# Performance work log

Hardware: AMD Instinct MI355X
Metric: run time of the kernel (lower is better)

Reference implementation:

```python
import jax, jax.numpy as jnp
import numpy as np

# dims: M=512 new tokens, N=2048 model dim, D=128 head dim, H=16 heads,
# L=4096 cache length, P=2048 cache write offset

def setup_inputs() -> dict:
    key = jax.random.key(0)
    k0, k1, k2, k3 = jax.random.split(key, 4)
    M, N, D, L = 512, 2048, 128, 4096
    X = jax.random.normal(k0, (M, N), jnp.float32)
    # scale weights ~1/sqrt(N) so projections have unit-ish scale
    W_qkv = jax.random.normal(k1, (N, 3 * N), jnp.float32) * (N ** -0.5)
    H = N // D
    cache_K = jax.random.normal(k2, (H, L, D), jnp.float32)
    # realistic cache state: keys stored in cache are RMS-normalized
    cache_K = cache_K * jax.lax.rsqrt(jnp.mean(cache_K * cache_K, axis=-1, keepdims=True))
    cache_V = jax.random.normal(k3, (H, L, D), jnp.float32)
    return {"X": X, "W_qkv": W_qkv, "cache_K": cache_K, "cache_V": cache_V, "P": 2048}


def reference(X, W_qkv, cache_K, cache_V, P):
    M = X.shape[0]
    H, L, D = cache_K.shape
    qkv = X @ W_qkv                              # [M, 3N]
    q, k, v = jnp.split(qkv, 3, axis=-1)         # each [M, N]
    q = q.reshape(M, H, D).transpose(1, 0, 2)    # [H, M, D]
    k = k.reshape(M, H, D).transpose(1, 0, 2)
    v = v.reshape(M, H, D).transpose(1, 0, 2)
    # RMS-style normalization (no learned gain, no eps in original)
    q = q * jax.lax.rsqrt(jnp.mean(q * q, axis=-1, keepdims=True))
    k = k * jax.lax.rsqrt(jnp.mean(k * k, axis=-1, keepdims=True))
    # scatter-update into KV cache at position P
    Kc = jax.lax.dynamic_update_slice(cache_K, k, (0, P, 0))  # [H, L, D]
    Vc = jax.lax.dynamic_update_slice(cache_V, v, (0, P, 0))
    # unmasked, unscaled attention over the full cache (faithful to original:
    # plain exp/sum, no max-subtraction, no 1/sqrt(D))
    scores = jnp.einsum('hmd,hld->hml', q, Kc)   # [H, M, L]
    w = jnp.exp(scores)
    w = w / jnp.sum(w, axis=-1, keepdims=True)
    out = jnp.einsum('hml,hld->hmd', w, Vc)      # [H, M, D]
    return out.transpose(1, 0, 2).reshape(M, H * D)
```

## Files before the change

### kernel.cpp

```cpp
#include <hip/hip_runtime.h>
#include <math.h>

typedef _Float16 half_t;
typedef _Float16 half8 __attribute__((ext_vector_type(8)));
typedef _Float16 half4_t __attribute__((ext_vector_type(4)));
typedef _Float16 half2_t __attribute__((ext_vector_type(2)));
typedef float floatx4 __attribute__((ext_vector_type(4)));

#define M_TOK 512
#define N_DIM 2048
#define D_HEAD 128
#define H_HEADS 16
#define L_CACHE 4096
#define THREE_N 6144
#define NCHUNK 8
#define LCHUNK 512

__global__ __launch_bounds__(256) void prep_kernel(const float* __restrict__ cK,
                                                   const float* __restrict__ cV,
                                                   const float* __restrict__ W,
                                                   const float* __restrict__ X,
                                                   const int* __restrict__ Pp,
                                                   half_t* __restrict__ K16,
                                                   half_t* __restrict__ V16T,
                                                   half_t* __restrict__ W16T,
                                                   half_t* __restrict__ X16) {
    __shared__ half_t tile[64 * 66];
    int b = blockIdx.x;
    int t = threadIdx.x;

    if (b < 4096) {
        int l0 = (b & 255) * 16;
        const int P = *Pp;
        if (l0 >= P && l0 + 16 <= P + M_TOK) return;
        size_t i = (size_t)b * 2048 + t * 4;
        float4 v0 = *(const float4*)(cK + i);
        float4 v1 = *(const float4*)(cK + i + 1024);
        half4_t h0 = {(half_t)v0.x, (half_t)v0.y, (half_t)v0.z, (half_t)v0.w};
        half4_t h1 = {(half_t)v1.x, (half_t)v1.y, (half_t)v1.z, (half_t)v1.w};
        *(half4_t*)(K16 + i) = h0;
        *(half4_t*)(K16 + i + 1024) = h1;
        return;
    }
    b -= 4096;
    if (b < 512) {
        size_t i = (size_t)b * 2048 + t * 4;
        float4 v0 = *(const float4*)(X + i);
        float4 v1 = *(const float4*)(X + i + 1024);
        half4_t h0 = {(half_t)v0.x, (half_t)v0.y, (half_t)v0.z, (half_t)v0.w};
        half4_t h1 = {(half_t)v1.x, (half_t)v1.y, (half_t)v1.z, (half_t)v1.w};
        *(half4_t*)(X16 + i) = h0;
        *(half4_t*)(X16 + i + 1024) = h1;
        return;
    }
    b -= 512;
    if (b < 2048) {
        int h = b >> 7;
        int rem = b & 127;
        int lt = rem >> 1, dt = rem & 1;
        int l0 = lt * 64, d0 = dt * 64;
        const int P = *Pp;
        if (l0 >= P && l0 + 64 <= P + M_TOK) return;
        {
            int l = t >> 2, c0 = (t & 3) * 16;
            const float* src = cV + ((size_t)h * L_CACHE + l0 + l) * D_HEAD + d0 + c0;
            float4 v[4];
#pragma unroll
            for (int j = 0; j < 4; ++j) v[j] = *(const float4*)(src + j * 4);
#pragma unroll
            for (int j = 0; j < 4; ++j) {
                tile[(c0 + j * 4 + 0) * 66 + l] = (half_t)v[j].x;
                tile[(c0 + j * 4 + 1) * 66 + l] = (half_t)v[j].y;
                tile[(c0 + j * 4 + 2) * 66 + l] = (half_t)v[j].z;
                tile[(c0 + j * 4 + 3) * 66 + l] = (half_t)v[j].w;
            }
        }
        __syncthreads();
        {
            int d = t >> 2, lg = (t & 3) * 16;
            half_t* dst = V16T + ((size_t)h * D_HEAD + d0 + d) * L_CACHE + l0 + lg;
            *(half8*)(dst) = *(half8*)&tile[d * 66 + lg];
            *(half8*)(dst + 8) = *(half8*)&tile[d * 66 + lg + 8];
        }
        return;
    }
    b -= 2048;
    {
        int n0 = (b % 96) * 64, k0 = (b / 96) * 64;
        {
            int k = t >> 2, c0 = (t & 3) * 16;
            const float* src = W + (size_t)(k0 + k) * THREE_N + n0 + c0;
            float4 v[4];
#pragma unroll
            for (int j = 0; j < 4; ++j) v[j] = *(const float4*)(src + j * 4);
#pragma unroll
            for (int j = 0; j < 4; ++j) {
                tile[(c0 + j * 4 + 0) * 66 + k] = (half_t)v[j].x;
                tile[(c0 + j * 4 + 1) * 66 + k] = (half_t)v[j].y;
                tile[(c0 + j * 4 + 2) * 66 + k] = (half_t)v[j].z;
                tile[(c0 + j * 4 + 3) * 66 + k] = (half_t)v[j].w;
            }
        }
        __syncthreads();
        {
            int n = t >> 2, kg = (t & 3) * 16;
            half_t* dst = W16T + (size_t)(n0 + n) * N_DIM + k0 + kg;
            *(half8*)(dst) = *(half8*)&tile[n * 66 + kg];
            *(half8*)(dst + 8) = *(half8*)&tile[n * 66 + kg + 8];
        }
    }
}

__global__ __launch_bounds__(256) void gemm_fused_kernel(const half_t* __restrict__ X16,
                                                         const half_t* __restrict__ W16T,
                                                         const int* __restrict__ Pp,
                                                         half_t* __restrict__ Q16,
                                                         half_t* __restrict__ K16,
                                                         half_t* __restrict__ V16T) {
    __shared__ half_t As[64 * 72];
    __shared__ half_t Bs[128 * 72];
    __shared__ half_t Vt[128 * 72];
    __shared__ float ssbuf[4][32];
    const int t = threadIdx.x;
    const int wid = t >> 6, lane = t & 63;
    const int quad = lane >> 4, ln = lane & 15;
    const int bx = blockIdx.x, by = blockIdx.y;
    const int m0 = by * 64, n0 = bx * 128;
    const int wm = (wid >> 1) * 32, wn = (wid & 1) * 64;

    floatx4 acc[2][4] = {};

    const int ar = t >> 3, ag = (t & 7) * 8;
    const int br = t >> 3, bg = (t & 7) * 8;

    for (int k0 = 0; k0 < N_DIM; k0 += 64) {
        __syncthreads();
#pragma unroll
        for (int p = 0; p < 2; ++p) {
            int r = ar + p * 32;
            *(half8*)&As[r * 72 + ag] =
                *(const half8*)(X16 + (size_t)(m0 + r) * N_DIM + k0 + ag);
        }
#pragma unroll
        for (int p = 0; p < 4; ++p) {
            int r = br + p * 32;
            *(half8*)&Bs[r * 72 + bg] =
                *(const half8*)(W16T + (size_t)(n0 + r) * N_DIM + k0 + bg);
        }
        __syncthreads();
#pragma unroll
        for (int kt = 0; kt < 2; ++kt) {
            half8 a[2], b[4];
#pragma unroll
            for (int i = 0; i < 2; ++i)
                a[i] = *(half8*)&As[(wm + i * 16 + ln) * 72 + kt * 32 + quad * 8];
#pragma unroll
            for (int j = 0; j < 4; ++j)
                b[j] = *(half8*)&Bs[(wn + j * 16 + ln) * 72 + kt * 32 + quad * 8];
#pragma unroll
            for (int i = 0; i < 2; ++i)
#pragma unroll
                for (int j = 0; j < 4; ++j)
                    acc[i][j] = __builtin_amdgcn_mfma_f32_16x16x32_f16(a[i], b[j], acc[i][j], 0, 0, 0);
        }
    }

    const int seg = bx >> 4, h = bx & 15;
    const int P = *Pp;

    if (seg < 2) {
        float ss[2][4], scale[2][4];
#pragma unroll
        for (int i = 0; i < 2; ++i)
#pragma unroll
            for (int r = 0; r < 4; ++r) {
                float s = 0.f;
#pragma unroll
                for (int j = 0; j < 4; ++j) s += acc[i][j][r] * acc[i][j][r];
#pragma unroll
                for (int msk = 1; msk < 16; msk <<= 1) s += __shfl_xor(s, msk, 64);
                ss[i][r] = s;
            }
        if (ln == 0) {
#pragma unroll
            for (int i = 0; i < 2; ++i)
#pragma unroll
                for (int r = 0; r < 4; ++r)
                    ssbuf[wid][i * 16 + quad * 4 + r] = ss[i][r];
        }
        __syncthreads();
#pragma unroll
        for (int i = 0; i < 2; ++i)
#pragma unroll
            for (int r = 0; r < 4; ++r)
                scale[i][r] =
                    rsqrtf((ss[i][r] + ssbuf[wid ^ 1][i * 16 + quad * 4 + r]) * (1.0f / 128.0f));
#pragma unroll
        for (int i = 0; i < 2; ++i) {
            int mbase = m0 + wm + i * 16 + quad * 4;
#pragma unroll
            for (int j = 0; j < 4; ++j) {
                int col = wn + j * 16 + ln;
#pragma unroll
                for (int r = 0; r < 4; ++r) {
                    int m = mbase + r;
                    half_t val = (half_t)(acc[i][j][r] * scale[i][r]);
                    if (seg == 0)
                        Q16[((size_t)h * M_TOK + m) * D_HEAD + col] = val;
                    else
                        K16[((size_t)h * L_CACHE + P + m) * D_HEAD + col] = val;
                }
            }
        }
    } else {
#pragma unroll
        for (int i = 0; i < 2; ++i) {
            int mbase = wm + i * 16 + quad * 4;
#pragma unroll
            for (int j = 0; j < 4; ++j) {
                int d = wn + j * 16 + ln;
#pragma unroll
                for (int r = 0; r < 4; ++r)
                    Vt[d * 72 + mbase + r] = (half_t)acc[i][j][r];
            }
        }
        __syncthreads();
#pragma unroll
        for (int p = 0; p < 4; ++p) {
            int s = p * 256 + t;
            int d = s >> 3, sg = s & 7;
            *(half8*)(V16T + ((size_t)h * D_HEAD + d) * L_CACHE + P + m0 + sg * 8) =
                *(half8*)&Vt[d * 72 + sg * 8];
        }
    }
}

__global__ __launch_bounds__(256, 4) void attn_partial_kernel(const half_t* __restrict__ Q16,
                                                              const half_t* __restrict__ K16,
                                                              const half_t* __restrict__ V16T,
                                                              half_t* __restrict__ Opart,
                                                              float* __restrict__ mstat,
                                                              float* __restrict__ lstat) {
    __shared__ half_t Ks[64 * 128];
    __shared__ half_t Vs[128 * 64];
    __shared__ half_t Ps[4 * 16 * 64];
    const int t = threadIdx.x, w = t >> 6, lane = t & 63;
    const int quad = lane >> 4, ln = lane & 15;

    const int bid = blockIdx.x;
    const int xcd = bid & 7, slot = bid >> 3;
    const int pair = (xcd << 4) | (slot >> 3);
    const int h = pair & 15, c = pair >> 4, mi = slot & 7;
    const int mb = mi * 64;

    const half_t* Qh = Q16 + (size_t)h * M_TOK * D_HEAD;
    const half_t* Kh = K16 + (size_t)h * L_CACHE * D_HEAD;
    const half_t* Vh = V16T + (size_t)h * D_HEAD * L_CACHE;

    const int m0 = mb + w * 16;
    half8 qf[4];
#pragma unroll
    for (int dt = 0; dt < 4; ++dt)
        qf[dt] = *(const half8*)(Qh + (size_t)(m0 + ln) * D_HEAD + dt * 32 + quad * 8);

    floatx4 oacc[8] = {};
    float mrow = -INFINITY;
    float lrow = 0.f;

    half_t* Pw = Ps + w * (16 * 64);
    const int psw = (ln & 7) << 3;

    const int l0base = c * LCHUNK;
    const int kr = t >> 4, kc = (t & 15) * 8;
    const int vr = t >> 3, vc = (t & 7) * 8;
    const int ksw = (kr & 7) << 3;
    const int vsw = (vr & 7) << 3;

    half8 kreg[4], vreg[4];
#pragma unroll
    for (int p = 0; p < 4; ++p) {
        kreg[p] = *(const half8*)(Kh + (size_t)(l0base + p * 16 + kr) * D_HEAD + kc);
        vreg[p] = *(const half8*)(Vh + (size_t)(p * 32 + vr) * L_CACHE + l0base + vc);
    }

    for (int it = 0; it < LCHUNK / 64; ++it) {
        __syncthreads();
#pragma unroll
        for (int p = 0; p < 4; ++p)
            *(half8*)&Ks[(p * 16 + kr) * 128 + (kc ^ ksw)] = kreg[p];
#pragma unroll
        for (int p = 0; p < 4; ++p)
            *(half8*)&Vs[(p * 32 + vr) * 64 + (vc ^ vsw)] = vreg[p];
        if (it + 1 < LCHUNK / 64) {
            int l1 = l0base + (it + 1) * 64;
#pragma unroll
            for (int p = 0; p < 4; ++p) {
                kreg[p] = *(const half8*)(Kh + (size_t)(l1 + p * 16 + kr) * D_HEAD + kc);
                vreg[p] = *(const half8*)(Vh + (size_t)(p * 32 + vr) * L_CACHE + l1 + vc);
            }
        }
        __syncthreads();

        floatx4 sacc[4] = {};
#pragma unroll
        for (int dt = 0; dt < 4; ++dt) {
            half8 kf[4];
#pragma unroll
            for (int nt = 0; nt < 4; ++nt)
                kf[nt] = *(half8*)&Ks[(nt * 16 + ln) * 128 + ((dt * 32 + quad * 8) ^ psw)];
#pragma unroll
            for (int nt = 0; nt < 4; ++nt)
                sacc[nt] = __builtin_amdgcn_mfma_f32_16x16x32_f16(kf[nt], qf[dt], sacc[nt], 0, 0, 0);
        }

        {
            float mx = sacc[0][0];
#pragma unroll
            for (int nt = 0; nt < 4; ++nt)
#pragma unroll
                for (int r = 0; r < 4; ++r) mx = fmaxf(mx, sacc[nt][r]);
            mx = fmaxf(mx, __shfl_xor(mx, 16));
            mx = fmaxf(mx, __shfl_xor(mx, 32));
            if (__ballot(mx > mrow)) {
                float mnew = fmaxf(mrow, mx);
                float alpha = __expf(mrow - mnew);
                mrow = mnew;
                lrow *= alpha;
                float ar[4];
#pragma unroll
                for (int r = 0; r < 4; ++r) ar[r] = __shfl(alpha, quad * 4 + r, 16);
#pragma unroll
                for (int nt8 = 0; nt8 < 8; ++nt8)
#pragma unroll
                    for (int r = 0; r < 4; ++r) oacc[nt8][r] *= ar[r];
            }
            float psum = 0.f;
#pragma unroll
            for (int nt = 0; nt < 4; ++nt) {
                half4_t h4;
#pragma unroll
                for (int r = 0; r < 4; ++r) {
                    float p = __expf(sacc[nt][r] - mrow);
                    psum += p;
                    h4[r] = (half_t)p;
                }
                *(half4_t*)&Pw[ln * 64 + ((nt * 16 + quad * 4) ^ psw)] = h4;
            }
            psum += __shfl_xor(psum, 16);
            psum += __shfl_xor(psum, 32);
            lrow += psum;
        }

#pragma unroll
        for (int kt = 0; kt < 2; ++kt) {
            half8 a = *(half8*)&Pw[ln * 64 + ((kt * 32 + quad * 8) ^ psw)];
#pragma unroll
            for (int nt8 = 0; nt8 < 8; ++nt8) {
                half8 b = *(half8*)&Vs[(nt8 * 16 + ln) * 64 + ((kt * 32 + quad * 8) ^ psw)];
                oacc[nt8] = __builtin_amdgcn_mfma_f32_16x16x32_f16(a, b, oacc[nt8], 0, 0, 0);
            }
        }
    }

    half_t* Oc = Opart + ((size_t)(c * H_HEADS + h) * M_TOK) * D_HEAD;
    float* ms = mstat + (size_t)(c * H_HEADS + h) * M_TOK;
    float* ls = lstat + (size_t)(c * H_HEADS + h) * M_TOK;
#pragma unroll
    for (int nt8 = 0; nt8 < 8; ++nt8) {
        int col = nt8 * 16 + ln;
#pragma unroll
        for (int r = 0; r < 4; ++r)
            Oc[(size_t)(m0 + quad * 4 + r) * D_HEAD + col] = (half_t)oacc[nt8][r];
    }
    if (lane < 16) {
        ms[m0 + lane] = mrow;
        ls[m0 + lane] = lrow;
    }
}

__global__ __launch_bounds__(256) void combine_kernel(const half_t* __restrict__ Opart,
                                                      const float* __restrict__ mstat,
                                                      const float* __restrict__ lstat,
                                                      float* __restrict__ out) {
    int gw = blockIdx.x * 4 + (threadIdx.x >> 6);
    int lane = threadIdx.x & 63;
    int h = gw >> 9, m = gw & 511;
    int d = lane * 2;

    float ms[NCHUNK];
    float mg = -INFINITY;
#pragma unroll
    for (int c = 0; c < NCHUNK; ++c) {
        ms[c] = mstat[((c * H_HEADS + h) << 9) + m];
        mg = fmaxf(mg, ms[c]);
    }
    float denom = 0.f, o0 = 0.f, o1 = 0.f;
#pragma unroll
    for (int c = 0; c < NCHUNK; ++c) {
        float e = __expf(ms[c] - mg);
        denom += lstat[((c * H_HEADS + h) << 9) + m] * e;
        const half_t* Oc = Opart + (((size_t)(c * H_HEADS + h) << 9) + m) * D_HEAD + d;
        half2_t v = *(const half2_t*)Oc;
        o0 += (float)v.x * e;
        o1 += (float)v.y * e;
    }
    float inv = 1.0f / denom;
    float* op = out + (size_t)m * N_DIM + h * D_HEAD + d;
    op[0] = o0 * inv;
    op[1] = o1 * inv;
}

extern "C" void kernel_launch(void* const* d_in, const int* in_sizes, int n_in,
                              void* d_out, int out_size, void* d_ws, size_t ws_size,
                              hipStream_t stream) {
    const float* X = (const float*)d_in[0];
    const float* W = (const float*)d_in[1];
    const float* cK = (const float*)d_in[2];
    const float* cV = (const float*)d_in[3];
    const int* Pp = (const int*)d_in[4];
    float* out = (float*)d_out;

    char* ws = (char*)d_ws;
    half_t* Q16 = (half_t*)(ws + 0);
    half_t* K16 = (half_t*)(ws + 2097152);
    half_t* V16T = (half_t*)(ws + 18874368);
    half_t* X16 = (half_t*)(ws + 35651584);
    half_t* W16T = (half_t*)(ws + 37748736);
    half_t* Opart = (half_t*)(ws + 37748736);
    float* mstat = (float*)(ws + 71303168);
    float* lstat = (float*)(ws + 71827456);

    prep_kernel<<<9728, 256, 0, stream>>>(cK, cV, W, X, Pp, K16, V16T, W16T, X16);
    gemm_fused_kernel<<<dim3(48, 8), 256, 0, stream>>>(X16, W16T, Pp, Q16, K16, V16T);
    attn_partial_kernel<<<1024, 256, 0, stream>>>(Q16, K16, V16T, Opart, mstat, lstat);
    combine_kernel<<<2048, 256, 0, stream>>>(Opart, mstat, lstat, out);
}
```

Before: 222.1 us.

## Move KV-cache fp16 conversion into GEMM launch to overlap with projection

Cache K/V conversion blocks move from the prep kernel into a combined kernel alongside the QKV GEMM blocks. GEMM blocks come first in block order and the cache-conversion blocks follow, so the bandwidth-bound conversion can overlap with the compute-bound GEMM instead of serialising ahead of it. Tiles that overlap the write window P..P+M are now masked per row or element so they do not overwrite the fresh K/V that the GEMM writes concurrently. The merged kernel uses a larger shared-memory footprint for every block, which may reduce occupancy for the conversion blocks.

```diff
diff --git a/kernel.cpp b/kernel.cpp
--- a/kernel.cpp
+++ b/kernel.cpp
@@ -16,34 +16,41 @@
 #define NCHUNK 8
 #define LCHUNK 512
 
-__global__ __launch_bounds__(256) void prep_kernel(const float* __restrict__ cK,
-                                                   const float* __restrict__ cV,
-                                                   const float* __restrict__ W,
+__global__ __launch_bounds__(256) void prep_kernel(const float* __restrict__ W,
                                                    const float* __restrict__ X,
-                                                   const int* __restrict__ Pp,
-                                                   half_t* __restrict__ K16,
-                                                   half_t* __restrict__ V16T,
                                                    half_t* __restrict__ W16T,
                                                    half_t* __restrict__ X16) {
     __shared__ half_t tile[64 * 66];
     int b = blockIdx.x;
     int t = threadIdx.x;
 
-    if (b < 4096) {
-        int l0 = (b & 255) * 16;
-        const int P = *Pp;
-        if (l0 >= P && l0 + 16 <= P + M_TOK) return;
-        size_t i = (size_t)b * 2048 + t * 4;
-        float4 v0 = *(const float4*)(cK + i);
-        float4 v1 = *(const float4*)(cK + i + 1024);
-        half4_t h0 = {(half_t)v0.x, (half_t)v0.y, (half_t)v0.z, (half_t)v0.w};
-        half4_t h1 = {(half_t)v1.x, (half_t)v1.y, (half_t)v1.z, (half_t)v1.w};
-        *(half4_t*)(K16 + i) = h0;
-        *(half4_t*)(K16 + i + 1024) = h1;
+    if (b < 3072) {
+        int n0 = (b % 96) * 64, k0 = (b / 96) * 64;
+        {
+            int k = t >> 2, c0 = (t & 3) * 16;
+            const float* src = W + (size_t)(k0 + k) * THREE_N + n0 + c0;
+            float4 v[4];
+#pragma unroll
+            for (int j = 0; j < 4; ++j) v[j] = *(const float4*)(src + j * 4);
+#pragma unroll
+            for (int j = 0; j < 4; ++j) {
+                tile[(c0 + j * 4 + 0) * 66 + k] = (half_t)v[j].x;
+                tile[(c0 + j * 4 + 1) * 66 + k] = (half_t)v[j].y;
+                tile[(c0 + j * 4 + 2) * 66 + k] = (half_t)v[j].z;
+                tile[(c0 + j * 4 + 3) * 66 + k] = (half_t)v[j].w;
+            }
+        }
+        __syncthreads();
+        {
+            int n = t >> 2, kg = (t & 3) * 16;
+            half_t* dst = W16T + (size_t)(n0 + n) * N_DIM + k0 + kg;
+            *(half8*)(dst) = *(half8*)&tile[n * 66 + kg];
+            *(half8*)(dst + 8) = *(half8*)&tile[n * 66 + kg + 8];
+        }
         return;
     }
-    b -= 4096;
-    if (b < 512) {
+    b -= 3072;
+    {
         size_t i = (size_t)b * 2048 + t * 4;
         float4 v0 = *(const float4*)(X + i);
         float4 v1 = *(const float4*)(X + i + 1024);
@@ -51,80 +58,86 @@
         half4_t h1 = {(half_t)v1.x, (half_t)v1.y, (half_t)v1.z, (half_t)v1.w};
         *(half4_t*)(X16 + i) = h0;
         *(half4_t*)(X16 + i + 1024) = h1;
-        return;
-    }
-    b -= 512;
-    if (b < 2048) {
-        int h = b >> 7;
-        int rem = b & 127;
-        int lt = rem >> 1, dt = rem & 1;
-        int l0 = lt * 64, d0 = dt * 64;
+    }
+}
+
+__global__ __launch_bounds__(256) void mega_kernel(const half_t* __restrict__ X16,
+                                                   const half_t* __restrict__ W16T,
+                                                   const float* __restrict__ cK,
+                                                   const float* __restrict__ cV,
+                                                   const int* __restrict__ Pp,
+                                                   half_t* __restrict__ Q16,
+                                                   half_t* __restrict__ K16,
+                                                   half_t* __restrict__ V16T) {
+    __shared__ __align__(16) char smem[46592];
+    const int t = threadIdx.x;
+    int b = blockIdx.x;
+
+    if (b >= 384) {
+        b -= 384;
         const int P = *Pp;
-        if (l0 >= P && l0 + 64 <= P + M_TOK) return;
+        if (b < 4096) {
+            int l0 = (b & 255) * 16;
+            if (l0 >= P && l0 + 16 <= P + M_TOK) return;
+            size_t i = (size_t)b * 2048 + t * 4;
+            int r0 = l0 + (t >> 5), r1 = r0 + 8;
+            float4 v0 = *(const float4*)(cK + i);
+            float4 v1 = *(const float4*)(cK + i + 1024);
+            half4_t h0 = {(half_t)v0.x, (half_t)v0.y, (half_t)v0.z, (half_t)v0.w};
+            half4_t h1 = {(half_t)v1.x, (half_t)v1.y, (half_t)v1.z, (half_t)v1.w};
+            if (r0 < P || r0 >= P + M_TOK) *(half4_t*)(K16 + i) = h0;
+            if (r1 < P || r1 >= P + M_TOK) *(half4_t*)(K16 + i + 1024) = h1;
+            return;
+        }
+        b -= 4096;
         {
-            int l = t >> 2, c0 = (t & 3) * 16;
-            const float* src = cV + ((size_t)h * L_CACHE + l0 + l) * D_HEAD + d0 + c0;
-            float4 v[4];
-#pragma unroll
-            for (int j = 0; j < 4; ++j) v[j] = *(const float4*)(src + j * 4);
-#pragma unroll
-            for (int j = 0; j < 4; ++j) {
-                tile[(c0 + j * 4 + 0) * 66 + l] = (half_t)v[j].x;
-                tile[(c0 + j * 4 + 1) * 66 + l] = (half_t)v[j].y;
-                tile[(c0 + j * 4 + 2) * 66 + l] = (half_t)v[j].z;
-                tile[(c0 + j * 4 + 3) * 66 + l] = (half_t)v[j].w;
-            }
-        }
-        __syncthreads();
-        {
-            int d = t >> 2, lg = (t & 3) * 16;
-            half_t* dst = V16T + ((size_t)h * D_HEAD + d0 + d) * L_CACHE + l0 + lg;
-            *(half8*)(dst) = *(half8*)&tile[d * 66 + lg];
-            *(half8*)(dst + 8) = *(half8*)&tile[d * 66 + lg + 8];
-        }
-        return;
-    }
-    b -= 2048;
-    {
-        int n0 = (b % 96) * 64, k0 = (b / 96) * 64;
-        {
-            int k = t >> 2, c0 = (t & 3) * 16;
-            const float* src = W + (size_t)(k0 + k) * THREE_N + n0 + c0;
-            float4 v[4];
-#pragma unroll
-            for (int j = 0; j < 4; ++j) v[j] = *(const float4*)(src + j * 4);
-#pragma unroll
-            for (int j = 0; j < 4; ++j) {
-                tile[(c0 + j * 4 + 0) * 66 + k] = (half_t)v[j].x;
-                tile[(c0 + j * 4 + 1) * 66 + k] = (half_t)v[j].y;
-                tile[(c0 + j * 4 + 2) * 66 + k] = (half_t)v[j].z;
-                tile[(c0 + j * 4 + 3) * 66 + k] = (half_t)v[j].w;
-            }
-        }
-        __syncthreads();
-        {
-            int n = t >> 2, kg = (t & 3) * 16;
-            half_t* dst = W16T + (size_t)(n0 + n) * N_DIM + k0 + kg;
-            *(half8*)(dst) = *(half8*)&tile[n * 66 + kg];
-            *(half8*)(dst + 8) = *(half8*)&tile[n * 66 + kg + 8];
-        }
-    }
-}
-
-__global__ __launch_bounds__(256) void gemm_fused_kernel(const half_t* __restrict__ X16,
-                                                         const half_t* __restrict__ W16T,
-                                                         const int* __restrict__ Pp,
-                                                         half_t* __restrict__ Q16,
-                                                         half_t* __restrict__ K16,
-                                                         half_t* __restrict__ V16T) {
-    __shared__ half_t As[64 * 72];
-    __shared__ half_t Bs[128 * 72];
-    __shared__ half_t Vt[128 * 72];
-    __shared__ float ssbuf[4][32];
-    const int t = threadIdx.x;
+            int h = b >> 7;
+            int rem = b & 127;
+            int lt = rem >> 1, dt = rem & 1;
+            int l0 = lt * 64, d0 = dt * 64;
+            if (l0 >= P && l0 + 64 <= P + M_TOK) return;
+            bool overlap = (l0 < P + M_TOK) && (l0 + 64 > P);
+            half_t* tile = (half_t*)smem;
+            {
+                int l = t >> 2, c0 = (t & 3) * 16;
+                const float* src = cV + ((size_t)h * L_CACHE + l0 + l) * D_HEAD + d0 + c0;
+                float4 v[4];
+#pragma unroll
+                for (int j = 0; j < 4; ++j) v[j] = *(const float4*)(src + j * 4);
+#pragma unroll
+                for (int j = 0; j < 4; ++j) {
+                    tile[(c0 + j * 4 + 0) * 66 + l] = (half_t)v[j].x;
+                    tile[(c0 + j * 4 + 1) * 66 + l] = (half_t)v[j].y;
+                    tile[(c0 + j * 4 + 2) * 66 + l] = (half_t)v[j].z;
+                    tile[(c0 + j * 4 + 3) * 66 + l] = (half_t)v[j].w;
+                }
+            }
+            __syncthreads();
+            {
+                int d = t >> 2, lg = (t & 3) * 16;
+                half_t* dst = V16T + ((size_t)h * D_HEAD + d0 + d) * L_CACHE + l0 + lg;
+                if (!overlap) {
+                    *(half8*)(dst) = *(half8*)&tile[d * 66 + lg];
+                    *(half8*)(dst + 8) = *(half8*)&tile[d * 66 + lg + 8];
+                } else {
+#pragma unroll
+                    for (int j = 0; j < 16; ++j) {
+                        int l = l0 + lg + j;
+                        if (l < P || l >= P + M_TOK) dst[j] = tile[d * 66 + lg + j];
+                    }
+                }
+            }
+            return;
+        }
+    }
+
+    half_t* As = (half_t*)smem;
+    half_t* Bs = (half_t*)(smem + 9216);
+    half_t* Vt = (half_t*)(smem + 27648);
+    float* ssb = (float*)(smem + 46080);
     const int wid = t >> 6, lane = t & 63;
     const int quad = lane >> 4, ln = lane & 15;
-    const int bx = blockIdx.x, by = blockIdx.y;
+    const int bx = b % 48, by = b / 48;
     const int m0 = by * 64, n0 = bx * 128;
     const int wm = (wid >> 1) * 32, wn = (wid & 1) * 64;
 
@@ -150,18 +163,18 @@
         __syncthreads();
 #pragma unroll
         for (int kt = 0; kt < 2; ++kt) {
-            half8 a[2], b[4];
+            half8 a[2], bb[4];
 #pragma unroll
             for (int i = 0; i < 2; ++i)
                 a[i] = *(half8*)&As[(wm + i * 16 + ln) * 72 + kt * 32 + quad * 8];
 #pragma unroll
             for (int j = 0; j < 4; ++j)
-                b[j] = *(half8*)&Bs[(wn + j * 16 + ln) * 72 + kt * 32 + quad * 8];
+                bb[j] = *(half8*)&Bs[(wn + j * 16 + ln) * 72 + kt * 32 + quad * 8];
 #pragma unroll
             for (int i = 0; i < 2; ++i)
 #pragma unroll
                 for (int j = 0; j < 4; ++j)
-                    acc[i][j] = __builtin_amdgcn_mfma_f32_16x16x32_f16(a[i], b[j], acc[i][j], 0, 0, 0);
+                    acc[i][j] = __builtin_amdgcn_mfma_f32_16x16x32_f16(a[i], bb[j], acc[i][j], 0, 0, 0);
         }
     }
 
@@ -186,7 +199,7 @@
             for (int i = 0; i < 2; ++i)
 #pragma unroll
                 for (int r = 0; r < 4; ++r)
-                    ssbuf[wid][i * 16 + quad * 4 + r] = ss[i][r];
+                    ssb[wid * 32 + i * 16 + quad * 4 + r] = ss[i][r];
         }
         __syncthreads();
 #pragma unroll
@@ -194,7 +207,7 @@
 #pragma unroll
             for (int r = 0; r < 4; ++r)
                 scale[i][r] =
-                    rsqrtf((ss[i][r] + ssbuf[wid ^ 1][i * 16 + quad * 4 + r]) * (1.0f / 128.0f));
+                    rsqrtf((ss[i][r] + ssb[(wid ^ 1) * 32 + i * 16 + quad * 4 + r]) * (1.0f / 128.0f));
 #pragma unroll
         for (int i = 0; i < 2; ++i) {
             int mbase = m0 + wm + i * 16 + quad * 4;
@@ -430,8 +443,8 @@
     float* mstat = (float*)(ws + 71303168);
     float* lstat = (float*)(ws + 71827456);
 
-    prep_kernel<<<9728, 256, 0, stream>>>(cK, cV, W, X, Pp, K16, V16T, W16T, X16);
-    gemm_fused_kernel<<<dim3(48, 8), 256, 0, stream>>>(X16, W16T, Pp, Q16, K16, V16T);
+    prep_kernel<<<3584, 256, 0, stream>>>(W, X, W16T, X16);
+    mega_kernel<<<6528, 256, 0, stream>>>(X16, W16T, cK, cV, Pp, Q16, K16, V16T);
     attn_partial_kernel<<<1024, 256, 0, stream>>>(Q16, K16, V16T, Opart, mstat, lstat);
     combine_kernel<<<2048, 256, 0, stream>>>(Opart, mstat, lstat, out);
 }
```

Result: faster. 212.4 us (-4.3%).
